# Kernel tuning notes

Hardware: AMD Instinct MI355X
Metric: run time of the kernel (lower is better)

The kernel has to match this reference:

```python
import jax, jax.numpy as jnp
import numpy as np

C = 128; HEADS = 8; GH = 32; GW = 32; B = 8; PD = 8  # PD = (dim//4)//4

def _conv(x, w, pad, dil=1, groups=1):
    return jax.lax.conv_general_dilated(
        x, w, (1, 1), [(pad[0], pad[0]), (pad[1], pad[1])],
        rhs_dilation=(dil, dil),
        dimension_numbers=('NCHW', 'OIHW', 'NCHW'),
        feature_group_count=groups)

def _lrelu(t):
    return jnp.where(t >= 0, t, 0.1 * t)

def _ln(t, g, b, eps=1e-5):
    m = jnp.mean(t, -1, keepdims=True)
    v = jnp.var(t, -1, keepdims=True)
    return (t - m) * jax.lax.rsqrt(v + eps) * g + b

def setup_inputs():
    rng = np.random.RandomState(0)
    f = lambda *s: jnp.asarray((rng.randn(*s) * 0.05).astype(np.float32))
    ones = lambda n: jnp.ones((n,), jnp.float32)
    zeros = lambda n: jnp.zeros((n,), jnp.float32)
    # Swin-style relative position index over the (GH, GW) group
    coords = np.stack(np.meshgrid(np.arange(GH), np.arange(GW), indexing='ij')).reshape(2, -1)
    rel = (coords[:, :, None] - coords[:, None, :]).transpose(1, 2, 0)
    rel[..., 0] += GH - 1; rel[..., 1] += GW - 1; rel[..., 0] *= 2 * GW - 1
    rel_idx = jnp.asarray(rel.sum(-1).astype(np.int32))  # [N, N]
    biases = np.stack(np.meshgrid(np.arange(1 - GH, GH), np.arange(1 - GW, GW), indexing='ij'))
    biases = jnp.asarray(biases.reshape(2, -1).T.astype(np.float32))  # [(2GH-1)*(2GW-1), 2]
    return dict(
        x=jnp.asarray(rng.rand(B, C, GH, GW).astype(np.float32)),
        conv1_w=f(C, C, 3, 3), conv2_w=f(C, C, 3, 3), conv3_w=f(C, C, 3, 3),
        convt_w=f(C, 3, 1, 1),
        rba_w=f(C, C, 3, 1), rba_b=zeros(C), rbb_w=f(C, C, 1, 3), rbb_b=zeros(C),
        pp_w=f(PD, 2), pp_b=zeros(PD),
        l1_g=ones(PD), l1_b=zeros(PD), l1_w=f(PD, PD), l1_b2=zeros(PD),
        l2_g=ones(PD), l2_b=zeros(PD), l2_w=f(PD, PD), l2_b2=zeros(PD),
        l3_g=ones(PD), l3_b=zeros(PD), l3_w=f(HEADS, PD), l3_b2=zeros(HEADS),
        qk_w=f(2 * C, C), qk_b=zeros(2 * C),
        v_w=f(C, C), v_b=zeros(C),
        proj_w=f(C, C), proj_b=zeros(C),
        fc1_w=f(C, C), fc1_b=zeros(C), fc2_w=f(C, C), fc2_b=zeros(C),
        biases=biases, rel_idx=rel_idx,
    )

def reference(x, conv1_w, conv2_w, conv3_w, convt_w, rba_w, rba_b, rbb_w, rbb_b,
              pp_w, pp_b, l1_g, l1_b, l1_w, l1_b2, l2_g, l2_b, l2_w, l2_b2,
              l3_g, l3_b, l3_w, l3_b2, qk_w, qk_b, v_w, v_b, proj_w, proj_b,
              fc1_w, fc1_b, fc2_w, fc2_b, biases, rel_idx):
    Bn, Cc, Hh, Ww = x.shape
    N = Hh * Ww
    hd = Cc // HEADS
    # FeaExtract: ResASPP (3 dilated 3x3 convs, grouped 1x1 merge) + residual
    b1 = _lrelu(_conv(x, conv1_w, (1, 1)))
    b2 = _lrelu(_conv(x, conv2_w, (3, 3), dil=3))
    b3 = _lrelu(_conv(x, conv3_w, (5, 5), dil=5))
    a = _conv(jnp.concatenate([b1, b2, b3], 1), convt_w, (0, 0), groups=Cc) + x
    # RB: (3,1) conv -> lrelu -> (1,3) conv + residual
    r = _lrelu(_conv(a, rba_w, (1, 0)) + rba_b[None, :, None, None])
    r = _conv(r, rbb_w, (0, 1)) + rbb_b[None, :, None, None]
    o0 = r + a
    # original uses in-place clamp_, so o0 is clamped before flattening
    o0 = jnp.clip(o0, 0.0, 1.0)
    E = o0.reshape(Bn, Cc, N).transpose(0, 2, 1)  # [B, N, C]
    qk = E @ qk_w.T + qk_b  # [B, N, 2C]
    q = qk[..., :Cc].reshape(Bn, N, HEADS, hd).transpose(0, 2, 1, 3)
    k = qk[..., Cc:].reshape(Bn, N, HEADS, hd).transpose(0, 2, 1, 3)
    v = (E @ v_w.T + v_b).reshape(Bn, N, HEADS, hd).transpose(0, 2, 1, 3)
    attn = jnp.einsum('bhid,bhjd->bhij', q * (hd ** -0.5), k)
    # DynamicPosBias MLP (residual=False): Linear(2,pd) -> [LN,ReLU,Linear] x2 -> LN,ReLU,Linear(pd,heads)
    p = biases @ pp_w.T + pp_b
    p = jax.nn.relu(_ln(p, l1_g, l1_b)) @ l1_w.T + l1_b2
    p = jax.nn.relu(_ln(p, l2_g, l2_b)) @ l2_w.T + l2_b2
    p = jax.nn.relu(_ln(p, l3_g, l3_b)) @ l3_w.T + l3_b2  # [L, heads]
    rpb = p[rel_idx]  # gather -> [N, N, heads]
    attn = attn + rpb.transpose(2, 0, 1)[None]
    attn = jax.nn.softmax(attn, axis=-1)
    y = jnp.einsum('bhij,bhjd->bhid', attn, v).transpose(0, 2, 1, 3).reshape(Bn, N, Cc) + E
    x_proj = y @ proj_w.T + proj_b
    h = jax.nn.gelu(x_proj @ fc1_w.T + fc1_b, approximate=False)
    return (h @ fc2_w.T + fc2_b) + y
```

## Files before the change

kernel.cpp:

```cpp
#include <hip/hip_runtime.h>
#include <hip/hip_bf16.h>

typedef __hip_bfloat16 bf16;
typedef __bf16 bf16x8 __attribute__((ext_vector_type(8)));
typedef float f32x4 __attribute__((ext_vector_type(4)));
typedef __fp16 f16x2 __attribute__((ext_vector_type(2)));
typedef __fp16 f16x4 __attribute__((ext_vector_type(4)));

#define Lb 3969
#define LOG2E 1.4426950408889634f
#define EXP2(x) __builtin_amdgcn_exp2f(x)

#define XP_F   0
#define WF_F   903168
#define WR_F   1124352
#define WG_F   1173504
#define BH_F   1222656
#define R1P_F  1222656
#define QKV_F  1222656
#define AP_F   2795520
#define YT_F   2795520
#define EB_F   3352576
#define XPT_F  3352576
#define H1T_F  0
#define RPB_F  3876864
#define FLAG_F 3908616
#define RT_F   3908624
#define VT_F   4924432

__device__ __forceinline__ float b2f(bf16 v) { return __bfloat162float(v); }
__device__ __forceinline__ bf16 f2b(float v) { return __float2bfloat16(v); }

template <typename T> __device__ __forceinline__ float ldw(const void* p, int i);
template <> __device__ __forceinline__ float ldw<bf16>(const void* p, int i) {
  return __bfloat162float(((const bf16*)p)[i]);
}
template <> __device__ __forceinline__ float ldw<float>(const void* p, int i) {
  return ((const float*)p)[i];
}
template <typename T> __device__ __forceinline__ void stw(void* p, size_t i, float v);
template <> __device__ __forceinline__ void stw<bf16>(void* p, size_t i, float v) {
  ((bf16*)p)[i] = __float2bfloat16(v);
}
template <> __device__ __forceinline__ void stw<float>(void* p, size_t i, float v) {
  ((float*)p)[i] = v;
}

__device__ __forceinline__ unsigned pkh(float a, float b) {
  f16x2 t = __builtin_amdgcn_cvt_pkrtz(a, b);
  return *(unsigned*)&t;
}

__device__ __forceinline__ bool detect_local(const unsigned* x) {
  int lane = threadIdx.x & 63;
  int cnt = 0;
#pragma unroll
  for (int k = 0; k < 4; ++k) {
    unsigned lo = x[lane + 64 * k] & 0xFFFFu;
    cnt += (lo >= 0x3C00u && lo < 0x3F80u) ? 1 : 0;
  }
#pragma unroll
  for (int off = 1; off < 64; off <<= 1) cnt += __shfl_xor(cnt, off);
  return cnt >= 128;
}

template <typename T>
__device__ void wprep_all_body(const void* w1, const void* w2, const void* w3,
                               const void* rba_w, const void* rbb_w,
                               const void* qk_w, const void* v_w,
                               const void* proj_w, const void* fc1_w,
                               const void* fc2_w, bf16* __restrict__ Wf,
                               bf16* __restrict__ Wr, bf16* __restrict__ Wg)
{
  int tid = blockIdx.x * 256 + threadIdx.x;
  int lane = tid & 63, li = lane & 15, quad = lane >> 4;
  if (tid < 55296) {
    int mt = (tid >> 6) & 7;
    int Kc = (tid >> 9) & 3;
    int rem = tid >> 11;
    int t = rem % 9;
    int br = rem / 9;
    const void* w = (br == 0 ? w1 : (br == 1 ? w2 : w3));
    int o = mt * 16 + li;
    int ci0 = Kc * 32 + quad * 8;
#pragma unroll
    for (int j = 0; j < 8; ++j)
      Wf[(size_t)tid * 8 + j] = f2b(ldw<T>(w, (o * 128 + ci0 + j) * 9 + t));
  } else {
    int u = tid - 55296;
    if (u < 12288) {
      int Kc = (u >> 6) & 3, mt = (u >> 8) & 7, q = u >> 11;
      const void* w = (q >= 3) ? rbb_w : rba_w;
      int t = q % 3;
#pragma unroll
      for (int j = 0; j < 8; ++j)
        Wr[(size_t)u * 8 + j] =
            f2b(ldw<T>(w, ((mt * 16 + li) * 128 + Kc * 32 + quad * 8 + j) * 3 + t));
    } else if (u < 24576) {
      int g = u - 12288;
      int Kc = (g >> 6) & 3, mtg = g >> 8;
      const void* w; int mrow; float sc = 1.f;
      if (mtg < 16)      { w = qk_w;   mrow = mtg * 16;
                           if (mtg < 8) sc = 0.25f * LOG2E; }
      else if (mtg < 24) { w = v_w;    mrow = (mtg - 16) * 16; }
      else if (mtg < 32) { w = proj_w; mrow = (mtg - 24) * 16; }
      else if (mtg < 40) { w = fc1_w;  mrow = (mtg - 32) * 16; }
      else               { w = fc2_w;  mrow = (mtg - 40) * 16; }
#pragma unroll
      for (int j = 0; j < 8; ++j)
        Wg[(size_t)g * 8 + j] =
            f2b(sc * ldw<T>(w, (mrow + li) * 128 + Kc * 32 + quad * 8 + j));
    }
  }
}

__global__ __launch_bounds__(256) void wprep_all_kernel(
    const unsigned* x, const void* w1, const void* w2, const void* w3,
    const void* rba_w, const void* rbb_w, const void* qk_w, const void* v_w,
    const void* proj_w, const void* fc1_w, const void* fc2_w,
    bf16* Wf, bf16* Wr, bf16* Wg, int* flag)
{
  bool isbf = detect_local(x);
  if (blockIdx.x == 0 && threadIdx.x == 0) *flag = isbf ? 1 : 0;
  if (isbf) wprep_all_body<bf16>(w1, w2, w3, rba_w, rbb_w, qk_w, v_w, proj_w,
                                 fc1_w, fc2_w, Wf, Wr, Wg);
  else      wprep_all_body<float>(w1, w2, w3, rba_w, rbb_w, qk_w, v_w, proj_w,
                                  fc1_w, fc2_w, Wf, Wr, Wg);
}

template <typename T>
__device__ void nhwc_body(const void* x, bf16* __restrict__ xp, bf16 (*tile)[128])
{
  const int b = blockIdx.x >> 5;
  const int row = blockIdx.x & 31;
  const int t = threadIdx.x;
  const size_t bbase = (size_t)b * 42 * 42 * 128;
  const bf16x8 z = (bf16x8){};

  if (t < 160) {
    int side = t / 80;
    int off = (t % 80) * 8;
    *(bf16x8*)&xp[bbase + ((size_t)(row + 5) * 42 + side * 37) * 128 + off] = z;
  }
  {
    int zr = (row < 5) ? row : ((row >= 27) ? row + 10 : -1);
    if (zr >= 0) {
      size_t base = bbase + (size_t)zr * 42 * 128;
      for (int k = t; k < 672; k += 256) *(bf16x8*)&xp[base + k * 8] = z;
    }
  }

  {
    int ci = t >> 1, half = t & 1;
#pragma unroll
    for (int j = 0; j < 16; ++j) {
      int px = half * 16 + j;
      tile[px][ci] = f2b(ldw<T>(x, ((size_t)b * 128 + ci) * 1024 + row * 32 + px));
    }
  }
  __syncthreads();
  {
    int px = t >> 3, c0 = (t & 7) * 16;
    bf16* dst = xp + (bbase + ((size_t)(row + 5) * 42 + (px + 5)) * 128 + c0);
#pragma unroll
    for (int j = 0; j < 16; ++j) dst[j] = tile[px][c0 + j];
  }
}

__global__ __launch_bounds__(256) void nhwc_kernel(const void* x, bf16* xp,
                                                   const int* flag)
{
  __shared__ bf16 tile[32][128];
  if (*flag) nhwc_body<bf16>(x, xp, tile);
  else       nhwc_body<float>(x, xp, tile);
}

__global__ __launch_bounds__(256) void aspp2_kernel(
    const bf16* __restrict__ xp, const bf16* __restrict__ Wf,
    bf16* __restrict__ bh)
{
  const int nt_ = blockIdx.x, br = blockIdx.y >> 1, mh = blockIdx.y & 1;
  const int bb = blockIdx.z;
  const int w = threadIdx.x >> 6, lane = threadIdx.x & 63;
  const int quad = lane >> 4, li = lane & 15;
  const int d = (br == 0 ? 1 : (br == 1 ? 3 : 5));
  const int pxw = nt_ * 64 + w * 16;
  const int y = pxw >> 5, xb = pxw & 31;

  f32x4 acc[4] = {};
  const bf16* Wbase = Wf + (size_t)br * 18432 * 8 + (size_t)mh * 4 * 64 * 8;

  for (int t = 0; t < 9; ++t) {
    const int dy = (t / 3 - 1) * d, dx = (t % 3 - 1) * d;
    const bf16* Asite =
        xp + (((size_t)bb * 42 + (y + 5 + dy)) * 42 + (xb + li + 5 + dx)) * 128;
    const bf16* Wt = Wbase + (size_t)t * 2048 * 8;
#pragma unroll
    for (int Kc = 0; Kc < 4; ++Kc) {
      bf16x8 afrag = *(const bf16x8*)(Asite + Kc * 32 + quad * 8);
      const bf16* Wk = Wt + (size_t)Kc * 512 * 8 + (size_t)lane * 8;
#pragma unroll
      for (int mt = 0; mt < 4; ++mt) {
        bf16x8 wfrag = *(const bf16x8*)(Wk + (size_t)mt * 64 * 8);
        acc[mt] = __builtin_amdgcn_mfma_f32_16x16x32_bf16(afrag, wfrag, acc[mt],
                                                          0, 0, 0);
      }
    }
  }
#pragma unroll
  for (int mt = 0; mt < 4; ++mt)
#pragma unroll
    for (int r = 0; r < 4; ++r) {
      int px = pxw + quad * 4 + r;
      bh[((size_t)bb * 1024 + px) * 384 + br * 128 + (mh * 4 + mt) * 16 + li] =
          f2b(acc[mt][r]);
    }
}

template <typename T>
__device__ void merge2_body(const bf16* __restrict__ xp, const void* wt,
                            const bf16* __restrict__ bh, bf16* __restrict__ ap,
                            float* cw)
{
  const int b = blockIdx.y, px0 = blockIdx.x * 32;
  const bf16x8 z = (bf16x8){};
  if (blockIdx.x == 0) {
    size_t base = ((size_t)b * 34 + 0) * 32 * 128;
    for (int k = threadIdx.x; k < 512; k += 256) *(bf16x8*)&ap[base + k * 8] = z;
  } else if (blockIdx.x == 31) {
    size_t base = ((size_t)b * 34 + 33) * 32 * 128;
    for (int k = threadIdx.x; k < 512; k += 256) *(bf16x8*)&ap[base + k * 8] = z;
  }
  for (int i = threadIdx.x; i < 384; i += 256) cw[i] = ldw<T>(wt, i);
  __syncthreads();
  const int pxl = threadIdx.x >> 3, og = threadIdx.x & 7;
  const int px = px0 + pxl, o0 = og * 16;
  const int y = px >> 5, x = px & 31;
  const bf16* brow = bh + ((size_t)b * 1024 + px) * 384 + o0 * 3;
  const bf16* xrow = xp + (((size_t)b * 42 + y + 5) * 42 + x + 5) * 128 + o0;
  bf16* arow = ap + (((size_t)b * 34 + y + 1) * 32 + x) * 128 + o0;

  bf16 bl[48], xl[16], ol[16];
#pragma unroll
  for (int k = 0; k < 6; ++k) *(bf16x8*)&bl[k * 8] = *(const bf16x8*)&brow[k * 8];
  *(bf16x8*)&xl[0] = *(const bf16x8*)&xrow[0];
  *(bf16x8*)&xl[8] = *(const bf16x8*)&xrow[8];
#pragma unroll
  for (int j = 0; j < 16; ++j) {
    float v = b2f(xl[j]);
#pragma unroll
    for (int i = 0; i < 3; ++i) {
      float t = b2f(bl[j * 3 + i]);
      v += cw[(o0 + j) * 3 + i] * (t >= 0.f ? t : 0.1f * t);
    }
    ol[j] = f2b(v);
  }
  *(bf16x8*)&arow[0] = *(bf16x8*)&ol[0];
  *(bf16x8*)&arow[8] = *(bf16x8*)&ol[8];
}

__global__ __launch_bounds__(256) void merge2_kernel(
    const bf16* xp, const void* wt, const bf16* bh, bf16* ap, const int* flag)
{
  __shared__ float cw[384];
  if (*flag) merge2_body<bf16>(xp, wt, bh, ap, cw);
  else       merge2_body<float>(xp, wt, bh, ap, cw);
}

template <typename T>
__device__ void rb1_body(const bf16* __restrict__ ap, const bf16* __restrict__ Wr,
                         const void* bias, bf16* __restrict__ r1p)
{
  const int b = blockIdx.z, mh = blockIdx.y;
  const int lane = threadIdx.x;
  const int quad = lane >> 4, li = lane & 15;
  const int pxw = blockIdx.x * 16;
  const int y = pxw >> 5, xb = pxw & 31;
  f32x4 acc[4] = {};
#pragma unroll
  for (int t = 0; t < 3; ++t) {
    const bf16* Asite = ap + (((size_t)b * 34 + y + t) * 32 + xb + li) * 128;
#pragma unroll
    for (int Kc = 0; Kc < 4; ++Kc) {
      bf16x8 afrag = *(const bf16x8*)(Asite + Kc * 32 + quad * 8);
#pragma unroll
      for (int mt = 0; mt < 4; ++mt) {
        int f = (t * 8 + mh * 4 + mt) * 4 + Kc;
        bf16x8 wfrag = *(const bf16x8*)(Wr + ((size_t)f * 64 + lane) * 8);
        acc[mt] = __builtin_amdgcn_mfma_f32_16x16x32_bf16(afrag, wfrag, acc[mt],
                                                          0, 0, 0);
      }
    }
  }
  if (quad == 0) {
    int xcol = (xb == 0) ? 0 : 33;
#pragma unroll
    for (int mt = 0; mt < 4; ++mt)
      r1p[(((size_t)b * 32 + y) * 34 + xcol) * 128 + (mh * 4 + mt) * 16 + li] =
          f2b(0.f);
  }
#pragma unroll
  for (int mt = 0; mt < 4; ++mt) {
    int o = (mh * 4 + mt) * 16 + li;
    float bv = ldw<T>(bias, o);
#pragma unroll
    for (int r = 0; r < 4; ++r) {
      int x = xb + quad * 4 + r;
      float v = acc[mt][r] + bv;
      v = (v >= 0.f ? v : 0.1f * v);
      r1p[(((size_t)b * 32 + y) * 34 + x + 1) * 128 + o] = f2b(v);
    }
  }
}

__global__ __launch_bounds__(64) void rb1_kernel(
    const bf16* ap, const bf16* Wr, const void* bias, bf16* r1p, const int* flag)
{
  if (*flag) rb1_body<bf16>(ap, Wr, bias, r1p);
  else       rb1_body<float>(ap, Wr, bias, r1p);
}

template <typename T>
__device__ void rb2_body(const bf16* __restrict__ r1p, const bf16* __restrict__ Wr,
                         const void* bias, const bf16* __restrict__ ap,
                         bf16* __restrict__ Eb)
{
  const int b = blockIdx.z, mh = blockIdx.y;
  const int lane = threadIdx.x;
  const int quad = lane >> 4, li = lane & 15;
  const int pxw = blockIdx.x * 16;
  const int y = pxw >> 5, xb = pxw & 31;
  f32x4 acc[4] = {};
#pragma unroll
  for (int t = 0; t < 3; ++t) {
    const bf16* Asite = r1p + (((size_t)b * 32 + y) * 34 + xb + li + t) * 128;
#pragma unroll
    for (int Kc = 0; Kc < 4; ++Kc) {
      bf16x8 afrag = *(const bf16x8*)(Asite + Kc * 32 + quad * 8);
#pragma unroll
      for (int mt = 0; mt < 4; ++mt) {
        int f = ((3 + t) * 8 + mh * 4 + mt) * 4 + Kc;
        bf16x8 wfrag = *(const bf16x8*)(Wr + ((size_t)f * 64 + lane) * 8);
        acc[mt] = __builtin_amdgcn_mfma_f32_16x16x32_bf16(afrag, wfrag, acc[mt],
                                                          0, 0, 0);
      }
    }
  }
#pragma unroll
  for (int mt = 0; mt < 4; ++mt) {
    int o = (mh * 4 + mt) * 16 + li;
    float bv = ldw<T>(bias, o);
#pragma unroll
    for (int r = 0; r < 4; ++r) {
      int x = xb + quad * 4 + r;
      float v = acc[mt][r] + bv +
                b2f(ap[(((size_t)b * 34 + y + 1) * 32 + x) * 128 + o]);
      v = fminf(fmaxf(v, 0.f), 1.f);
      Eb[((size_t)b * 1024 + y * 32 + x) * 128 + o] = f2b(v);
    }
  }
}

__global__ __launch_bounds__(64) void rb2_kernel(
    const bf16* r1p, const bf16* Wr, const void* bias, const bf16* ap,
    bf16* Eb, const int* flag)
{
  if (*flag) rb2_body<bf16>(r1p, Wr, bias, ap, Eb);
  else       rb2_body<float>(r1p, Wr, bias, ap, Eb);
}

template <typename T>
__device__ __forceinline__ void ln_relu8(const float* t, float* u,
                                         const void* g, const void* bb)
{
  float m = 0.f;
#pragma unroll
  for (int k = 0; k < 8; ++k) m += t[k];
  m *= 0.125f;
  float v = 0.f;
#pragma unroll
  for (int k = 0; k < 8; ++k) { float d = t[k] - m; v += d * d; }
  v *= 0.125f;
  float r = rsqrtf(v + 1e-5f);
#pragma unroll
  for (int k = 0; k < 8; ++k) {
    float val = (t[k] - m) * r * ldw<T>(g, k) + ldw<T>(bb, k);
    u[k] = val > 0.f ? val : 0.f;
  }
}

template <typename T>
__device__ void dpb_body(const void* biases, const void* pp_w, const void* pp_b,
                         const void* l1_g, const void* l1_b, const void* l1_w,
                         const void* l1_b2, const void* l2_g, const void* l2_b,
                         const void* l2_w, const void* l2_b2, const void* l3_g,
                         const void* l3_b, const void* l3_w, const void* l3_b2,
                         float* __restrict__ RPB)
{
  int r = blockIdx.x * 256 + threadIdx.x;
  if (r >= Lb) return;
  float b0 = ldw<T>(biases, r * 2), b1 = ldw<T>(biases, r * 2 + 1);
  float t[8], u[8];
#pragma unroll
  for (int j = 0; j < 8; ++j)
    t[j] = b0 * ldw<T>(pp_w, j * 2) + b1 * ldw<T>(pp_w, j * 2 + 1) +
           ldw<T>(pp_b, j);
  ln_relu8<T>(t, u, l1_g, l1_b);
#pragma unroll
  for (int j = 0; j < 8; ++j) {
    float s = ldw<T>(l1_b2, j);
#pragma unroll
    for (int k = 0; k < 8; ++k) s += u[k] * ldw<T>(l1_w, j * 8 + k);
    t[j] = s;
  }
  ln_relu8<T>(t, u, l2_g, l2_b);
#pragma unroll
  for (int j = 0; j < 8; ++j) {
    float s = ldw<T>(l2_b2, j);
#pragma unroll
    for (int k = 0; k < 8; ++k) s += u[k] * ldw<T>(l2_w, j * 8 + k);
    t[j] = s;
  }
  ln_relu8<T>(t, u, l3_g, l3_b);
#pragma unroll
  for (int h = 0; h < 8; ++h) {
    float s = ldw<T>(l3_b2, h);
#pragma unroll
    for (int k = 0; k < 8; ++k) s += u[k] * ldw<T>(l3_w, h * 8 + k);
    RPB[h * Lb + r] = s;
  }
}

__global__ __launch_bounds__(256) void dpb_kernel(
    const void* biases, const void* pp_w, const void* pp_b, const void* l1_g,
    const void* l1_b, const void* l1_w, const void* l1_b2, const void* l2_g,
    const void* l2_b, const void* l2_w, const void* l2_b2, const void* l3_g,
    const void* l3_b, const void* l3_w, const void* l3_b2, float* RPB,
    const int* flag)
{
  if (*flag)
    dpb_body<bf16>(biases, pp_w, pp_b, l1_g, l1_b, l1_w, l1_b2, l2_g, l2_b,
                   l2_w, l2_b2, l3_g, l3_b, l3_w, l3_b2, RPB);
  else
    dpb_body<float>(biases, pp_w, pp_b, l1_g, l1_b, l1_w, l1_b2, l2_g, l2_b,
                    l2_w, l2_b2, l3_g, l3_b, l3_w, l3_b2, RPB);
}

__global__ __launch_bounds__(64) void rt_kernel(
    const float* __restrict__ RPB, float* __restrict__ RTf)
{
  const int tt = blockIdx.x, h = blockIdx.y;
  const int t = tt >> 1, p = tt & 1;
  const int lane = threadIdx.x, quad = lane >> 4, li = lane & 15;
  const float* rp = RPB + h * Lb;
  float* dst = RTf + ((size_t)(h * 124 + tt) * 4) * 256 + lane * 4;
#pragma unroll
  for (int mt = 0; mt < 4; ++mt) {
    f32x4 v;
#pragma unroll
    for (int r = 0; r < 4; ++r) {
      int j = mt * 16 + quad * 4 + r;
      int dy = (t - 30) - (j >> 5);
      int dx = (p * 16 + li) - (j & 31);
      v[r] = rp[(dy + 31) * 63 + dx + 31] * LOG2E;
    }
    *(f32x4*)(dst + mt * 256) = v;
  }
}

__global__ __launch_bounds__(64) void vt_kernel(
    const bf16* __restrict__ QKV, uint2* __restrict__ VTh)
{
  const int c = blockIdx.x, hh = blockIdx.y, b = blockIdx.z;
  __shared__ bf16 Vl[64][20];
  const int lane = threadIdx.x, quad = lane >> 4, li = lane & 15;
  const bf16* vsrc =
      QKV + ((size_t)b * 1024 + c * 64 + lane) * 384 + 256 + hh * 16;
  union { bf16x8 v; uint2 u[2]; } w0, w1;
  w0.v = *(const bf16x8*)vsrc;
  w1.v = *(const bf16x8*)(vsrc + 8);
  *(uint2*)&Vl[lane][0] = w0.u[0];
  *(uint2*)&Vl[lane][4] = w0.u[1];
  *(uint2*)&Vl[lane][8] = w1.u[0];
  *(uint2*)&Vl[lane][12] = w1.u[1];
  __syncthreads();
  uint2* dst = VTh + (((size_t)(b * 8 + hh) * 16 + c) * 4) * 64 + lane;
#pragma unroll
  for (int mt = 0; mt < 4; ++mt) {
    uint2 pu;
    pu.x = pkh(b2f(Vl[mt * 16 + quad * 4 + 0][li]),
               b2f(Vl[mt * 16 + quad * 4 + 1][li]));
    pu.y = pkh(b2f(Vl[mt * 16 + quad * 4 + 2][li]),
               b2f(Vl[mt * 16 + quad * 4 + 3][li]));
    dst[(size_t)mt * 64] = pu;
  }
}

template <typename T>
__device__ void qkv_body(const bf16* __restrict__ Eb, const bf16* __restrict__ Wg,
                         const void* qk_b, const void* v_b,
                         bf16* __restrict__ QKV)
{
  const int grp = blockIdx.y, b = blockIdx.z;
  const int w = threadIdx.x >> 6, lane = threadIdx.x & 63;
  const int quad = lane >> 4, li = lane & 15;
  const int pxw = blockIdx.x * 64 + w * 16;
  bf16x8 ef[4];
#pragma unroll
  for (int Kc = 0; Kc < 4; ++Kc)
    ef[Kc] = *(const bf16x8*)&Eb[((size_t)b * 1024 + pxw + li) * 128 + Kc * 32 +
                                 quad * 8];
  f32x4 acc[8] = {};
#pragma unroll
  for (int nt = 0; nt < 8; ++nt) {
    int g = grp * 8 + nt;
#pragma unroll
    for (int Kc = 0; Kc < 4; ++Kc) {
      bf16x8 wf = *(const bf16x8*)&Wg[(((size_t)g * 4 + Kc) * 64 + lane) * 8];
      acc[nt] = __builtin_amdgcn_mfma_f32_16x16x32_bf16(ef[Kc], wf, acc[nt],
                                                        0, 0, 0);
    }
  }
#pragma unroll
  for (int nt = 0; nt < 8; ++nt) {
    int g = grp * 8 + nt;
    int o = g * 16 + li;
    float bv;
    if (g < 8)       bv = (0.25f * LOG2E) * ldw<T>(qk_b, o);
    else if (g < 16) bv = ldw<T>(qk_b, o);
    else             bv = ldw<T>(v_b, o - 256);
#pragma unroll
    for (int r = 0; r < 4; ++r) {
      int px = pxw + quad * 4 + r;
      QKV[((size_t)b * 1024 + px) * 384 + o] = f2b(acc[nt][r] + bv);
    }
  }
}

__global__ __launch_bounds__(256) void qkv_kernel(
    const bf16* Eb, const bf16* Wg, const void* qk_b, const void* v_b,
    bf16* QKV, const int* flag)
{
  if (*flag) qkv_body<bf16>(Eb, Wg, qk_b, v_b, QKV);
  else       qkv_body<float>(Eb, Wg, qk_b, v_b, QKV);
}

template <typename T, int MODE>
__device__ void mlp_body(const bf16* __restrict__ src, const bf16* __restrict__ Wg,
                         int tb, const void* bias, const bf16* __restrict__ res,
                         void* out)
{
  const int b = blockIdx.z, mh = blockIdx.y;
  const int lane = threadIdx.x;
  const int quad = lane >> 4, li = lane & 15;
  const int pxw = blockIdx.x * 16;
  bf16x8 ef[4];
#pragma unroll
  for (int Kc = 0; Kc < 4; ++Kc)
    ef[Kc] = *(const bf16x8*)&src[((size_t)b * 1024 + pxw + li) * 128 + Kc * 32 +
                                  quad * 8];
  f32x4 acc[2] = {};
#pragma unroll
  for (int nt = 0; nt < 2; ++nt)
#pragma unroll
    for (int Kc = 0; Kc < 4; ++Kc) {
      bf16x8 wf = *(const bf16x8*)&Wg[
          (((size_t)(tb + mh * 2 + nt) * 4 + Kc) * 64 + lane) * 8];
      acc[nt] = __builtin_amdgcn_mfma_f32_16x16x32_bf16(ef[Kc], wf, acc[nt],
                                                        0, 0, 0);
    }
#pragma unroll
  for (int nt = 0; nt < 2; ++nt) {
    int o = (mh * 2 + nt) * 16 + li;
    float bv = ldw<T>(bias, o);
#pragma unroll
    for (int r = 0; r < 4; ++r) {
      int px = pxw + quad * 4 + r;
      float v = acc[nt][r] + bv;
      size_t oidx = ((size_t)b * 1024 + px) * 128 + o;
      if (MODE == 1) v = 0.5f * v * (1.f + erff(v * 0.70710678118f));
      if (MODE == 2) {
        v += b2f(res[oidx]);
        stw<T>(out, oidx, v);
      } else {
        ((bf16*)out)[oidx] = f2b(v);
      }
    }
  }
}

template <int MODE>
__global__ __launch_bounds__(64) void mlp_kernel(
    const bf16* src, const bf16* Wg, int tb, const void* bias, const bf16* res,
    void* out, const int* flag)
{
  if (*flag) mlp_body<bf16, MODE>(src, Wg, tb, bias, res, out);
  else       mlp_body<float, MODE>(src, Wg, tb, bias, res, out);
}

__global__ __launch_bounds__(256, 4) void attn_kernel(
    const bf16* __restrict__ QKV, const bf16* __restrict__ Eb,
    const float* __restrict__ RTf, const uint2* __restrict__ VTh,
    bf16* __restrict__ Yt)
{
  const int qt = blockIdx.x * 4 + (threadIdx.x >> 6);
  const int hh = blockIdx.y;
  const int b = blockIdx.z;

  const int lane = threadIdx.x & 63;
  const int quad = lane >> 4, li = lane & 15;
  const int qb = qt * 16;

  const bf16* QKVb = QKV + (size_t)b * 1024 * 384;
  const uint2* VTb = VTh + (size_t)(b * 8 + hh) * 4096;
  const float* RTh = RTf + (size_t)hh * 124 * 1024;

  bf16x8 qf = (bf16x8){};
  if (quad < 2)
    qf = *(const bf16x8*)&QKVb[(size_t)(qb + li) * 384 + hh * 16 + quad * 8];

  f32x4 Oa = {}, Ob = {};
  float m_st = -1e30f, l_ln = 0.f;
  const int sbase = (lane & 48) + ((lane >> 2) & 12);

  struct Buf { bf16x8 kf[4]; f32x4 cin[4]; uint2 vb[4]; };
  Buf bA, bB;

  auto LOAD = [&](Buf& bf, int c) {
    const int c0 = c * 64;
    const int tt = ((qt >> 1) - 2 * c + 30) * 2 + (qt & 1);
    const float* rtp = RTh + (size_t)tt * 1024 + lane * 4;
#pragma unroll
    for (int mt = 0; mt < 4; ++mt) {
      bf.cin[mt] = *(const f32x4*)(rtp + mt * 256);
      bf.kf[mt] = (bf16x8){};
      if (quad < 2)
        bf.kf[mt] = *(const bf16x8*)&QKVb[(size_t)(c0 + mt * 16 + li) * 384 +
                                          128 + hh * 16 + quad * 8];
      bf.vb[mt] = VTb[(size_t)(c * 4 + mt) * 64 + lane];
    }
  };

  auto STEP = [&](const Buf& bf) {
    f32x4 sT[4];
#pragma unroll
    for (int mt = 0; mt < 4; ++mt)
      sT[mt] = __builtin_amdgcn_mfma_f32_16x16x32_bf16(bf.kf[mt], qf,
                                                       bf.cin[mt], 0, 0, 0);

    float m0 = fmaxf(fmaxf(sT[0][0], sT[0][1]), fmaxf(sT[0][2], sT[0][3]));
    float m1 = fmaxf(fmaxf(sT[1][0], sT[1][1]), fmaxf(sT[1][2], sT[1][3]));
    float m2 = fmaxf(fmaxf(sT[2][0], sT[2][1]), fmaxf(sT[2][2], sT[2][3]));
    float m3 = fmaxf(fmaxf(sT[3][0], sT[3][1]), fmaxf(sT[3][2], sT[3][3]));
    float lmax = fmaxf(fmaxf(m0, m1), fmaxf(m2, m3));

    if (!__all(lmax <= m_st + 11.5f)) {
      float cm = fmaxf(lmax, __shfl_xor(lmax, 16));
      cm = fmaxf(cm, __shfl_xor(cm, 32));
      float mn = fmaxf(m_st, cm);
      float al = EXP2(m_st - mn);
      m_st = mn;
      l_ln *= al;
#pragma unroll
      for (int r = 0; r < 4; ++r) {
        float a = __shfl(al, sbase + r);
        Oa[r] *= a;
        Ob[r] *= a;
      }
    }

#pragma unroll
    for (int mt = 0; mt < 4; ++mt)
#pragma unroll
      for (int r = 0; r < 4; ++r) sT[mt][r] = EXP2(sT[mt][r] - m_st);

    float s0 = (sT[0][0] + sT[0][1]) + (sT[0][2] + sT[0][3]);
    float s1 = (sT[1][0] + sT[1][1]) + (sT[1][2] + sT[1][3]);
    float s2 = (sT[2][0] + sT[2][1]) + (sT[2][2] + sT[2][3]);
    float s3 = (sT[3][0] + sT[3][1]) + (sT[3][2] + sT[3][3]);
    l_ln += (s0 + s1) + (s2 + s3);

#pragma unroll
    for (int mt = 0; mt < 4; ++mt) {
      union { unsigned u[2]; f16x4 h4; } pu;
      pu.u[0] = pkh(sT[mt][0], sT[mt][1]);
      pu.u[1] = pkh(sT[mt][2], sT[mt][3]);
      union { uint2 u; f16x4 h; } vu;
      vu.u = bf.vb[mt];
      if (mt & 2)
        Ob = __builtin_amdgcn_mfma_f32_16x16x16f16(pu.h4, vu.h, Ob, 0, 0, 0);
      else
        Oa = __builtin_amdgcn_mfma_f32_16x16x16f16(pu.h4, vu.h, Oa, 0, 0, 0);
    }
  };

  LOAD(bA, 0);
  for (int c = 0; c < 16; c += 2) {
    LOAD(bB, c + 1);
    STEP(bA);
    if (c + 2 < 16) LOAD(bA, c + 2);
    STEP(bB);
  }

  float l_st = l_ln + __shfl_xor(l_ln, 16);
  l_st += __shfl_xor(l_st, 32);

  f32x4 O_;
#pragma unroll
  for (int r = 0; r < 4; ++r) O_[r] = Oa[r] + Ob[r];

  const bf16* Ebp = Eb + (size_t)b * 1024 * 128 + hh * 16 + li;
  bf16* Ytp = Yt + (size_t)b * 1024 * 128 + hh * 16 + li;
#pragma unroll
  for (int r = 0; r < 4; ++r) {
    float lb = __shfl(l_st, sbase + r);
    int qrow = qb + quad * 4 + r;
    Ytp[(size_t)qrow * 128] =
        f2b(O_[r] / lb + b2f(Ebp[(size_t)qrow * 128]));
  }
}

extern "C" void kernel_launch(void* const* d_in, const int* in_sizes, int n_in,
                              void* d_out, int out_size, void* d_ws,
                              size_t ws_size, hipStream_t stream)
{
  (void)in_sizes; (void)n_in; (void)out_size; (void)ws_size;
  const void* x       = d_in[0];
  const void* conv1_w = d_in[1];
  const void* conv2_w = d_in[2];
  const void* conv3_w = d_in[3];
  const void* convt_w = d_in[4];
  const void* rba_w   = d_in[5];
  const void* rba_b   = d_in[6];
  const void* rbb_w   = d_in[7];
  const void* rbb_b   = d_in[8];
  const void* pp_w    = d_in[9];
  const void* pp_b    = d_in[10];
  const void* l1_g    = d_in[11];
  const void* l1_b    = d_in[12];
  const void* l1_w    = d_in[13];
  const void* l1_b2   = d_in[14];
  const void* l2_g    = d_in[15];
  const void* l2_b    = d_in[16];
  const void* l2_w    = d_in[17];
  const void* l2_b2   = d_in[18];
  const void* l3_g    = d_in[19];
  const void* l3_b    = d_in[20];
  const void* l3_w    = d_in[21];
  const void* l3_b2   = d_in[22];
  const void* qk_w    = d_in[23];
  const void* qk_b    = d_in[24];
  const void* v_w     = d_in[25];
  const void* v_b     = d_in[26];
  const void* proj_w  = d_in[27];
  const void* proj_b  = d_in[28];
  const void* fc1_w   = d_in[29];
  const void* fc1_b   = d_in[30];
  const void* fc2_w   = d_in[31];
  const void* fc2_b   = d_in[32];
  const void* biases  = d_in[33];

  float* ws   = (float*)d_ws;
  bf16*  xp   = (bf16*)(ws + XP_F);
  bf16*  Wf   = (bf16*)(ws + WF_F);
  bf16*  Wr   = (bf16*)(ws + WR_F);
  bf16*  Wg   = (bf16*)(ws + WG_F);
  bf16*  bh   = (bf16*)(ws + BH_F);
  bf16*  r1p  = (bf16*)(ws + R1P_F);
  bf16*  QKV  = (bf16*)(ws + QKV_F);
  bf16*  ap   = (bf16*)(ws + AP_F);
  bf16*  Yt   = (bf16*)(ws + YT_F);
  bf16*  Eb   = (bf16*)(ws + EB_F);
  bf16*  XPt  = (bf16*)(ws + XPT_F);
  bf16*  H1t  = (bf16*)(ws + H1T_F);
  float* RPB  = ws + RPB_F;
  int*   flag = (int*)(ws + FLAG_F);
  float* RTf  = ws + RT_F;
  uint2* VTh  = (uint2*)(ws + VT_F);

  wprep_all_kernel<<<312, 256, 0, stream>>>(
      (const unsigned*)x, conv1_w, conv2_w, conv3_w, rba_w, rbb_w, qk_w, v_w,
      proj_w, fc1_w, fc2_w, Wf, Wr, Wg, flag);
  nhwc_kernel<<<256, 256, 0, stream>>>(x, xp, flag);
  aspp2_kernel<<<dim3(16, 6, 8), 256, 0, stream>>>(xp, Wf, bh);
  merge2_kernel<<<dim3(32, 8), 256, 0, stream>>>(xp, convt_w, bh, ap, flag);
  rb1_kernel<<<dim3(64, 2, 8), 64, 0, stream>>>(ap, Wr, rba_b, r1p, flag);
  rb2_kernel<<<dim3(64, 2, 8), 64, 0, stream>>>(r1p, Wr, rbb_b, ap, Eb, flag);
  dpb_kernel<<<16, 256, 0, stream>>>(biases, pp_w, pp_b, l1_g, l1_b, l1_w,
                                     l1_b2, l2_g, l2_b, l2_w, l2_b2, l3_g,
                                     l3_b, l3_w, l3_b2, RPB, flag);
  rt_kernel<<<dim3(124, 8), 64, 0, stream>>>(RPB, RTf);
  qkv_kernel<<<dim3(16, 3, 8), 256, 0, stream>>>(Eb, Wg, qk_b, v_b, QKV, flag);
  vt_kernel<<<dim3(16, 8, 8), 64, 0, stream>>>(QKV, VTh);
  attn_kernel<<<dim3(16, 8, 8), 256, 0, stream>>>(QKV, Eb, RTf, VTh, Yt);
  mlp_kernel<0><<<dim3(64, 4, 8), 64, 0, stream>>>(Yt, Wg, 24, proj_b, nullptr,
                                                   XPt, flag);
  mlp_kernel<1><<<dim3(64, 4, 8), 64, 0, stream>>>(XPt, Wg, 32, fc1_b, nullptr,
                                                   H1t, flag);
  mlp_kernel<2><<<dim3(64, 4, 8), 64, 0, stream>>>(H1t, Wg, 40, fc2_b, Yt,
                                                   d_out, flag);
}
```

Before: 249.6 us.

## Fuse prep kernels, write V transpose from QKV epilogue, fuse MLP chain

After: 233.0 us. 1.07x faster.

```diff
diff --git a/kernel.cpp b/kernel.cpp
--- a/kernel.cpp
+++ b/kernel.cpp
@@ -21,8 +21,6 @@
 #define AP_F   2795520
 #define YT_F   2795520
 #define EB_F   3352576
-#define XPT_F  3352576
-#define H1T_F  0
 #define RPB_F  3876864
 #define FLAG_F 3908616
 #define RT_F   3908624
@@ -114,25 +112,12 @@
   }
 }
 
-__global__ __launch_bounds__(256) void wprep_all_kernel(
-    const unsigned* x, const void* w1, const void* w2, const void* w3,
-    const void* rba_w, const void* rbb_w, const void* qk_w, const void* v_w,
-    const void* proj_w, const void* fc1_w, const void* fc2_w,
-    bf16* Wf, bf16* Wr, bf16* Wg, int* flag)
-{
-  bool isbf = detect_local(x);
-  if (blockIdx.x == 0 && threadIdx.x == 0) *flag = isbf ? 1 : 0;
-  if (isbf) wprep_all_body<bf16>(w1, w2, w3, rba_w, rbb_w, qk_w, v_w, proj_w,
-                                 fc1_w, fc2_w, Wf, Wr, Wg);
-  else      wprep_all_body<float>(w1, w2, w3, rba_w, rbb_w, qk_w, v_w, proj_w,
-                                  fc1_w, fc2_w, Wf, Wr, Wg);
-}
-
 template <typename T>
-__device__ void nhwc_body(const void* x, bf16* __restrict__ xp, bf16 (*tile)[128])
-{
-  const int b = blockIdx.x >> 5;
-  const int row = blockIdx.x & 31;
+__device__ void nhwc_body(const void* x, bf16* __restrict__ xp,
+                          bf16 (*tile)[128], int bid)
+{
+  const int b = bid >> 5;
+  const int row = bid & 31;
   const int t = threadIdx.x;
   const size_t bbase = (size_t)b * 42 * 42 * 128;
   const bf16x8 z = (bf16x8){};
@@ -167,12 +152,25 @@
   }
 }
 
-__global__ __launch_bounds__(256) void nhwc_kernel(const void* x, bf16* xp,
-                                                   const int* flag)
+__global__ __launch_bounds__(256) void prep_kernel(
+    const unsigned* x, const void* w1, const void* w2, const void* w3,
+    const void* rba_w, const void* rbb_w, const void* qk_w, const void* v_w,
+    const void* proj_w, const void* fc1_w, const void* fc2_w,
+    bf16* Wf, bf16* Wr, bf16* Wg, bf16* xp, int* flag)
 {
   __shared__ bf16 tile[32][128];
-  if (*flag) nhwc_body<bf16>(x, xp, tile);
-  else       nhwc_body<float>(x, xp, tile);
+  bool isbf = detect_local(x);
+  if (blockIdx.x < 312) {
+    if (blockIdx.x == 0 && threadIdx.x == 0) *flag = isbf ? 1 : 0;
+    if (isbf) wprep_all_body<bf16>(w1, w2, w3, rba_w, rbb_w, qk_w, v_w, proj_w,
+                                   fc1_w, fc2_w, Wf, Wr, Wg);
+    else      wprep_all_body<float>(w1, w2, w3, rba_w, rbb_w, qk_w, v_w, proj_w,
+                                    fc1_w, fc2_w, Wf, Wr, Wg);
+  } else {
+    int bid = blockIdx.x - 312;
+    if (isbf) nhwc_body<bf16>(x, xp, tile, bid);
+    else      nhwc_body<float>(x, xp, tile, bid);
+  }
 }
 
 __global__ __launch_bounds__(256) void aspp2_kernel(
@@ -468,38 +466,10 @@
   }
 }
 
-__global__ __launch_bounds__(64) void vt_kernel(
-    const bf16* __restrict__ QKV, uint2* __restrict__ VTh)
-{
-  const int c = blockIdx.x, hh = blockIdx.y, b = blockIdx.z;
-  __shared__ bf16 Vl[64][20];
-  const int lane = threadIdx.x, quad = lane >> 4, li = lane & 15;
-  const bf16* vsrc =
-      QKV + ((size_t)b * 1024 + c * 64 + lane) * 384 + 256 + hh * 16;
-  union { bf16x8 v; uint2 u[2]; } w0, w1;
-  w0.v = *(const bf16x8*)vsrc;
-  w1.v = *(const bf16x8*)(vsrc + 8);
-  *(uint2*)&Vl[lane][0] = w0.u[0];
-  *(uint2*)&Vl[lane][4] = w0.u[1];
-  *(uint2*)&Vl[lane][8] = w1.u[0];
-  *(uint2*)&Vl[lane][12] = w1.u[1];
-  __syncthreads();
-  uint2* dst = VTh + (((size_t)(b * 8 + hh) * 16 + c) * 4) * 64 + lane;
-#pragma unroll
-  for (int mt = 0; mt < 4; ++mt) {
-    uint2 pu;
-    pu.x = pkh(b2f(Vl[mt * 16 + quad * 4 + 0][li]),
-               b2f(Vl[mt * 16 + quad * 4 + 1][li]));
-    pu.y = pkh(b2f(Vl[mt * 16 + quad * 4 + 2][li]),
-               b2f(Vl[mt * 16 + quad * 4 + 3][li]));
-    dst[(size_t)mt * 64] = pu;
-  }
-}
-
 template <typename T>
 __device__ void qkv_body(const bf16* __restrict__ Eb, const bf16* __restrict__ Wg,
                          const void* qk_b, const void* v_b,
-                         bf16* __restrict__ QKV)
+                         bf16* __restrict__ QKV, uint2* __restrict__ VTh)
 {
   const int grp = blockIdx.y, b = blockIdx.z;
   const int w = threadIdx.x >> 6, lane = threadIdx.x & 63;
@@ -521,81 +491,138 @@
                                                         0, 0, 0);
     }
   }
-#pragma unroll
-  for (int nt = 0; nt < 8; ++nt) {
-    int g = grp * 8 + nt;
-    int o = g * 16 + li;
-    float bv;
-    if (g < 8)       bv = (0.25f * LOG2E) * ldw<T>(qk_b, o);
-    else if (g < 16) bv = ldw<T>(qk_b, o);
-    else             bv = ldw<T>(v_b, o - 256);
-#pragma unroll
-    for (int r = 0; r < 4; ++r) {
-      int px = pxw + quad * 4 + r;
-      QKV[((size_t)b * 1024 + px) * 384 + o] = f2b(acc[nt][r] + bv);
+  if (grp < 2) {
+#pragma unroll
+    for (int nt = 0; nt < 8; ++nt) {
+      int g = grp * 8 + nt;
+      int o = g * 16 + li;
+      float bv = (g < 8) ? (0.25f * LOG2E) * ldw<T>(qk_b, o) : ldw<T>(qk_b, o);
+#pragma unroll
+      for (int r = 0; r < 4; ++r) {
+        int px = pxw + quad * 4 + r;
+        QKV[((size_t)b * 1024 + px) * 384 + o] = f2b(acc[nt][r] + bv);
+      }
+    }
+  } else {
+#pragma unroll
+    for (int nt = 0; nt < 8; ++nt) {
+      int hh = nt;
+      float bv = ldw<T>(v_b, nt * 16 + li);
+      uint2 pu;
+      pu.x = pkh(acc[nt][0] + bv, acc[nt][1] + bv);
+      pu.y = pkh(acc[nt][2] + bv, acc[nt][3] + bv);
+      VTh[(((size_t)(b * 8 + hh) * 16 + blockIdx.x) * 4 + w) * 64 + lane] = pu;
     }
   }
 }
 
 __global__ __launch_bounds__(256) void qkv_kernel(
     const bf16* Eb, const bf16* Wg, const void* qk_b, const void* v_b,
-    bf16* QKV, const int* flag)
-{
-  if (*flag) qkv_body<bf16>(Eb, Wg, qk_b, v_b, QKV);
-  else       qkv_body<float>(Eb, Wg, qk_b, v_b, QKV);
-}
-
-template <typename T, int MODE>
-__device__ void mlp_body(const bf16* __restrict__ src, const bf16* __restrict__ Wg,
-                         int tb, const void* bias, const bf16* __restrict__ res,
-                         void* out)
-{
-  const int b = blockIdx.z, mh = blockIdx.y;
-  const int lane = threadIdx.x;
+    bf16* QKV, uint2* VTh, const int* flag)
+{
+  if (*flag) qkv_body<bf16>(Eb, Wg, qk_b, v_b, QKV, VTh);
+  else       qkv_body<float>(Eb, Wg, qk_b, v_b, QKV, VTh);
+}
+
+template <typename T>
+__device__ void mlpf_body(const bf16* __restrict__ Yt, const bf16* __restrict__ Wg,
+                          const void* proj_b, const void* fc1_b,
+                          const void* fc2_b, void* out,
+                          bf16 (*buf0)[136], bf16 (*buf1)[136])
+{
+  const int w = threadIdx.x >> 6, lane = threadIdx.x & 63;
   const int quad = lane >> 4, li = lane & 15;
-  const int pxw = blockIdx.x * 16;
+  const size_t row0 = (size_t)blockIdx.x * 16;
+
   bf16x8 ef[4];
+  f32x4 acc[2];
+
 #pragma unroll
   for (int Kc = 0; Kc < 4; ++Kc)
-    ef[Kc] = *(const bf16x8*)&src[((size_t)b * 1024 + pxw + li) * 128 + Kc * 32 +
-                                  quad * 8];
-  f32x4 acc[2] = {};
-#pragma unroll
-  for (int nt = 0; nt < 2; ++nt)
+    ef[Kc] = *(const bf16x8*)&Yt[(row0 + li) * 128 + Kc * 32 + quad * 8];
+  acc[0] = (f32x4){}; acc[1] = (f32x4){};
+#pragma unroll
+  for (int j = 0; j < 2; ++j) {
+    int g = 24 + w * 2 + j;
 #pragma unroll
     for (int Kc = 0; Kc < 4; ++Kc) {
-      bf16x8 wf = *(const bf16x8*)&Wg[
-          (((size_t)(tb + mh * 2 + nt) * 4 + Kc) * 64 + lane) * 8];
-      acc[nt] = __builtin_amdgcn_mfma_f32_16x16x32_bf16(ef[Kc], wf, acc[nt],
-                                                        0, 0, 0);
-    }
-#pragma unroll
-  for (int nt = 0; nt < 2; ++nt) {
-    int o = (mh * 2 + nt) * 16 + li;
-    float bv = ldw<T>(bias, o);
+      bf16x8 wf = *(const bf16x8*)&Wg[(((size_t)g * 4 + Kc) * 64 + lane) * 8];
+      acc[j] = __builtin_amdgcn_mfma_f32_16x16x32_bf16(ef[Kc], wf, acc[j],
+                                                       0, 0, 0);
+    }
+  }
+#pragma unroll
+  for (int j = 0; j < 2; ++j) {
+    int o = (w * 2 + j) * 16 + li;
+    float bv = ldw<T>(proj_b, o);
+#pragma unroll
+    for (int r = 0; r < 4; ++r)
+      buf0[quad * 4 + r][o] = f2b(acc[j][r] + bv);
+  }
+  __syncthreads();
+
+#pragma unroll
+  for (int Kc = 0; Kc < 4; ++Kc)
+    ef[Kc] = *(const bf16x8*)&buf0[li][Kc * 32 + quad * 8];
+  acc[0] = (f32x4){}; acc[1] = (f32x4){};
+#pragma unroll
+  for (int j = 0; j < 2; ++j) {
+    int g = 32 + w * 2 + j;
+#pragma unroll
+    for (int Kc = 0; Kc < 4; ++Kc) {
+      bf16x8 wf = *(const bf16x8*)&Wg[(((size_t)g * 4 + Kc) * 64 + lane) * 8];
+      acc[j] = __builtin_amdgcn_mfma_f32_16x16x32_bf16(ef[Kc], wf, acc[j],
+                                                       0, 0, 0);
+    }
+  }
+#pragma unroll
+  for (int j = 0; j < 2; ++j) {
+    int o = (w * 2 + j) * 16 + li;
+    float bv = ldw<T>(fc1_b, o);
 #pragma unroll
     for (int r = 0; r < 4; ++r) {
-      int px = pxw + quad * 4 + r;
-      float v = acc[nt][r] + bv;
-      size_t oidx = ((size_t)b * 1024 + px) * 128 + o;
-      if (MODE == 1) v = 0.5f * v * (1.f + erff(v * 0.70710678118f));
-      if (MODE == 2) {
-        v += b2f(res[oidx]);
-        stw<T>(out, oidx, v);
-      } else {
-        ((bf16*)out)[oidx] = f2b(v);
-      }
-    }
-  }
-}
-
-template <int MODE>
-__global__ __launch_bounds__(64) void mlp_kernel(
-    const bf16* src, const bf16* Wg, int tb, const void* bias, const bf16* res,
-    void* out, const int* flag)
-{
-  if (*flag) mlp_body<bf16, MODE>(src, Wg, tb, bias, res, out);
-  else       mlp_body<float, MODE>(src, Wg, tb, bias, res, out);
+      float v = acc[j][r] + bv;
+      v = 0.5f * v * (1.f + erff(v * 0.70710678118f));
+      buf1[quad * 4 + r][o] = f2b(v);
+    }
+  }
+  __syncthreads();
+
+#pragma unroll
+  for (int Kc = 0; Kc < 4; ++Kc)
+    ef[Kc] = *(const bf16x8*)&buf1[li][Kc * 32 + quad * 8];
+  acc[0] = (f32x4){}; acc[1] = (f32x4){};
+#pragma unroll
+  for (int j = 0; j < 2; ++j) {
+    int g = 40 + w * 2 + j;
+#pragma unroll
+    for (int Kc = 0; Kc < 4; ++Kc) {
+      bf16x8 wf = *(const bf16x8*)&Wg[(((size_t)g * 4 + Kc) * 64 + lane) * 8];
+      acc[j] = __builtin_amdgcn_mfma_f32_16x16x32_bf16(ef[Kc], wf, acc[j],
+                                                       0, 0, 0);
+    }
+  }
+#pragma unroll
+  for (int j = 0; j < 2; ++j) {
+    int o = (w * 2 + j) * 16 + li;
+    float bv = ldw<T>(fc2_b, o);
+#pragma unroll
+    for (int r = 0; r < 4; ++r) {
+      size_t oidx = (row0 + quad * 4 + r) * 128 + o;
+      float v = acc[j][r] + bv + b2f(Yt[oidx]);
+      stw<T>(out, oidx, v);
+    }
+  }
+}
+
+__global__ __launch_bounds__(256) void mlpf_kernel(
+    const bf16* Yt, const bf16* Wg, const void* proj_b, const void* fc1_b,
+    const void* fc2_b, void* out, const int* flag)
+{
+  __shared__ bf16 buf0[16][136];
+  __shared__ bf16 buf1[16][136];
+  if (*flag) mlpf_body<bf16>(Yt, Wg, proj_b, fc1_b, fc2_b, out, buf0, buf1);
+  else       mlpf_body<float>(Yt, Wg, proj_b, fc1_b, fc2_b, out, buf0, buf1);
 }
 
 __global__ __launch_bounds__(256, 4) void attn_kernel(
@@ -771,17 +798,14 @@
   bf16*  ap   = (bf16*)(ws + AP_F);
   bf16*  Yt   = (bf16*)(ws + YT_F);
   bf16*  Eb   = (bf16*)(ws + EB_F);
-  bf16*  XPt  = (bf16*)(ws + XPT_F);
-  bf16*  H1t  = (bf16*)(ws + H1T_F);
   float* RPB  = ws + RPB_F;
   int*   flag = (int*)(ws + FLAG_F);
   float* RTf  = ws + RT_F;
   uint2* VTh  = (uint2*)(ws + VT_F);
 
-  wprep_all_kernel<<<312, 256, 0, stream>>>(
+  prep_kernel<<<568, 256, 0, stream>>>(
       (const unsigned*)x, conv1_w, conv2_w, conv3_w, rba_w, rbb_w, qk_w, v_w,
-      proj_w, fc1_w, fc2_w, Wf, Wr, Wg, flag);
-  nhwc_kernel<<<256, 256, 0, stream>>>(x, xp, flag);
+      proj_w, fc1_w, fc2_w, Wf, Wr, Wg, xp, flag);
   aspp2_kernel<<<dim3(16, 6, 8), 256, 0, stream>>>(xp, Wf, bh);
   merge2_kernel<<<dim3(32, 8), 256, 0, stream>>>(xp, convt_w, bh, ap, flag);
   rb1_kernel<<<dim3(64, 2, 8), 64, 0, stream>>>(ap, Wr, rba_b, r1p, flag);
@@ -790,13 +814,9 @@
                                      l1_b2, l2_g, l2_b, l2_w, l2_b2, l3_g,
                                      l3_b, l3_w, l3_b2, RPB, flag);
   rt_kernel<<<dim3(124, 8), 64, 0, stream>>>(RPB, RTf);
-  qkv_kernel<<<dim3(16, 3, 8), 256, 0, stream>>>(Eb, Wg, qk_b, v_b, QKV, flag);
-  vt_kernel<<<dim3(16, 8, 8), 64, 0, stream>>>(QKV, VTh);
+  qkv_kernel<<<dim3(16, 3, 8), 256, 0, stream>>>(Eb, Wg, qk_b, v_b, QKV, VTh,
+                                                 flag);
   attn_kernel<<<dim3(16, 8, 8), 256, 0, stream>>>(QKV, Eb, RTf, VTh, Yt);
-  mlp_kernel<0><<<dim3(64, 4, 8), 64, 0, stream>>>(Yt, Wg, 24, proj_b, nullptr,
-                                                   XPt, flag);
-  mlp_kernel<1><<<dim3(64, 4, 8), 64, 0, stream>>>(XPt, Wg, 32, fc1_b, nullptr,
-                                                   H1t, flag);
-  mlp_kernel<2><<<dim3(64, 4, 8), 64, 0, stream>>>(H1t, Wg, 40, fc2_b, Yt,
-                                                   d_out, flag);
-}
+  mlpf_kernel<<<512, 256, 0, stream>>>(Yt, Wg, proj_b, fc1_b, fc2_b, d_out,
+                                       flag);
+}
```
